# Performance work log

Measured on AMD Instinct MI355X. Metric: run time of the kernel, lower is better.

Reference implementation:

```python
import jax, jax.numpy as jnp
import numpy as np

N_NODES = 50000
N_EDGES = 800000
D_IN = 128
HIDDEN = 128
N_LAYERS = 3
N_CLASSES = 10
N_GRAPHS = 512
BN_EPS = 1e-5


def gcn_conv(x, edges, W, b):
    """PyG GCNConv: D^{-1/2}(A+I)D^{-1/2} X W + b (self-loops added)."""
    N = x.shape[0]
    src, dst = edges[0], edges[1]
    # degrees with self-loops
    deg = jax.ops.segment_sum(jnp.ones(src.shape[0], x.dtype), dst, num_segments=N) + 1.0
    dinv = jax.lax.rsqrt(deg)
    h = x @ W                                   # [N, out]
    norm = dinv[src] * dinv[dst]                # [E]
    out = jax.ops.segment_sum(h[src] * norm[:, None], dst, num_segments=N)
    out = out + h * (dinv * dinv)[:, None]      # self-loop messages
    return out + b


def batch_norm(x, gamma, beta):
    # BatchNorm1d in training mode: batch stats over node axis, biased var
    mu = x.mean(axis=0)
    var = x.var(axis=0)
    return gamma * (x - mu) * jax.lax.rsqrt(var + BN_EPS) + beta


def setup_inputs() -> dict:
    key = jax.random.key(0)
    ks = jax.random.split(key, 12)
    x = jax.random.normal(ks[0], (N_NODES, D_IN), dtype=jnp.float32)
    edges = jax.random.randint(ks[1], (2, N_EDGES), 0, N_NODES, dtype=jnp.int64)
    batch = jnp.sort(jax.random.randint(ks[2], (N_NODES,), 0, N_GRAPHS, dtype=jnp.int64))
    s_in = 1.0 / np.sqrt(D_IN)
    s_h = 1.0 / np.sqrt(HIDDEN)
    return {
        "x": x,
        "edges": edges,
        "batch": batch,
        "W1": jax.random.normal(ks[3], (D_IN, HIDDEN), dtype=jnp.float32) * s_in,
        "b1": jnp.zeros((HIDDEN,), jnp.float32),
        "g1": jnp.ones((HIDDEN,), jnp.float32),
        "be1": jnp.zeros((HIDDEN,), jnp.float32),
        "Wc": jax.random.normal(ks[4], (N_LAYERS, HIDDEN, HIDDEN), dtype=jnp.float32) * s_h,
        "bc": jnp.zeros((N_LAYERS, HIDDEN), jnp.float32),
        "gc": jnp.ones((N_LAYERS, HIDDEN), jnp.float32),
        "bec": jnp.zeros((N_LAYERS, HIDDEN), jnp.float32),
        "Wl": jax.random.normal(ks[5], (HIDDEN, N_CLASSES), dtype=jnp.float32) * s_h,
        "bl": jnp.zeros((N_CLASSES,), jnp.float32),
    }


def reference(x, edges, batch, W1, b1, g1, be1, Wc, bc, gc, bec, Wl, bl):
    h = jax.nn.relu(batch_norm(gcn_conv(x, edges, W1, b1), g1, be1))
    for i in range(N_LAYERS):  # fixed small layer loop
        h = jax.nn.relu(batch_norm(gcn_conv(h, edges, Wc[i], bc[i]), gc[i], bec[i]))
    # global_mean_pool over per-node graph ids
    sums = jax.ops.segment_sum(h, batch, num_segments=N_GRAPHS)
    counts = jax.ops.segment_sum(jnp.ones(h.shape[0], h.dtype), batch, num_segments=N_GRAPHS)
    pooled = sums / jnp.maximum(counts, 1.0)[:, None]
    return pooled @ Wl + bl
```

## Files before the change

kernel.cpp:

```cpp
#include <hip/hip_runtime.h>
#include <hip/hip_bf16.h>

#define NN 50000
#define NE 800000
#define DH 128
#define NGRAPH 512
#define NCLS 10
#define BN_EPS 1e-5f
#define SCAN_NB ((NN + 255) / 256)
#define GEMM_NB ((NN + 63) / 64)
#define BN1_NB 1024
#define BN2_NB 32
#define FILL_SEG 392
#define FILL_NB (FILL_SEG * 8)
#define STRIPE ((NN + 7) / 8)

typedef unsigned int uint;
typedef unsigned short ushort;
typedef __attribute__((ext_vector_type(8))) short short8;
typedef __attribute__((ext_vector_type(4))) float f32x4;

__device__ __forceinline__ ushort f2bf(float x) {
    __hip_bfloat16 h = __float2bfloat16(x);
    return *(ushort*)&h;
}
__device__ __forceinline__ float bf_lo(uint v) { return __uint_as_float(v << 16); }
__device__ __forceinline__ float bf_hi(uint v) { return __uint_as_float(v & 0xffff0000u); }


__launch_bounds__(256)
__global__ void hist_kernel(const int* __restrict__ dst, int* __restrict__ counts, int E) {
    int stripe = blockIdx.x & 7;
    int seg = blockIdx.x >> 3;
    int lo = stripe * STRIPE;
    int hi = lo + STRIPE;
    for (int e = seg * 256 + threadIdx.x; e < E; e += FILL_SEG * 256) {
        int d = dst[e];
        if (d >= lo && d < hi) atomicAdd(&counts[d], 1);
    }
}

__launch_bounds__(256)
__global__ void scan1_kernel(const int* __restrict__ counts, int* __restrict__ bsum, int N) {
    __shared__ int ls[256];
    int i = blockIdx.x * 256 + threadIdx.x;
    ls[threadIdx.x] = (i < N) ? counts[i] : 0;
    __syncthreads();
    for (int off = 128; off > 0; off >>= 1) {
        if (threadIdx.x < off) ls[threadIdx.x] += ls[threadIdx.x + off];
        __syncthreads();
    }
    if (threadIdx.x == 0) bsum[blockIdx.x] = ls[0];
}

__launch_bounds__(256)
__global__ void scan2_kernel(int* __restrict__ bsum, int NB) {
    __shared__ int ls[256];
    int tid = threadIdx.x;
    int v = (tid < NB) ? bsum[tid] : 0;
    ls[tid] = v;
    __syncthreads();
    for (int off = 1; off < 256; off <<= 1) {
        int t = (tid >= off) ? ls[tid - off] : 0;
        __syncthreads();
        ls[tid] += t;
        __syncthreads();
    }
    if (tid < NB) bsum[tid] = ls[tid] - v;
}

__launch_bounds__(256)
__global__ void scan3_kernel(const int* __restrict__ counts, const int* __restrict__ boff,
                             int* __restrict__ offsets, int* __restrict__ cursor,
                             float* __restrict__ dinv, int N) {
    __shared__ int ls[256];
    int tid = threadIdx.x;
    int i = blockIdx.x * 256 + tid;
    int v = (i < N) ? counts[i] : 0;
    ls[tid] = v;
    __syncthreads();
    for (int off = 1; off < 256; off <<= 1) {
        int t = (tid >= off) ? ls[tid - off] : 0;
        __syncthreads();
        ls[tid] += t;
        __syncthreads();
    }
    int base = boff[blockIdx.x];
    if (i < N) {
        int ex = base + ls[tid] - v;
        offsets[i] = ex;
        cursor[i] = ex;
        dinv[i] = rsqrtf((float)(v + 1));
        if (i == N - 1) offsets[N] = base + ls[tid];
    }
}

__launch_bounds__(256)
__global__ void fill_kernel(const int* __restrict__ src, const int* __restrict__ dst,
                            int* __restrict__ cursor, int* __restrict__ csr_src, int E) {
    int stripe = blockIdx.x & 7;
    int seg = blockIdx.x >> 3;
    int lo = stripe * STRIPE;
    int hi = lo + STRIPE;
    for (int e = seg * 256 + threadIdx.x; e < E; e += FILL_SEG * 256) {
        int d = dst[e];
        if (d >= lo && d < hi) {
            int pos = atomicAdd(&cursor[d], 1);
            csr_src[pos] = src[e];
        }
    }
}


__launch_bounds__(256)
__global__ void wtrans_kernel(const float* __restrict__ W1, const float* __restrict__ Wc,
                              ushort* __restrict__ WT) {
    int layer = blockIdx.x >> 4;
    int kt = (blockIdx.x >> 2) & 3, nt = blockIdx.x & 3;
    const float* W = (layer == 0) ? W1 : Wc + (size_t)(layer - 1) * DH * DH;
    __shared__ float tile[32][33];
    int t = threadIdx.x;
    int r = t >> 3;
    int c4 = (t & 7) * 4;
    float4 v = *(const float4*)&W[(size_t)(kt * 32 + r) * DH + nt * 32 + c4];
    tile[r][c4 + 0] = v.x; tile[r][c4 + 1] = v.y;
    tile[r][c4 + 2] = v.z; tile[r][c4 + 3] = v.w;
    __syncthreads();
    int n = t >> 3, k4 = (t & 7) * 4;
    ushort4 o;
    o.x = f2bf(tile[k4 + 0][n]);
    o.y = f2bf(tile[k4 + 1][n]);
    o.z = f2bf(tile[k4 + 2][n]);
    o.w = f2bf(tile[k4 + 3][n]);
    *(ushort4*)&WT[(size_t)layer * DH * DH + (size_t)(nt * 32 + n) * DH + kt * 32 + k4] = o;
}


template<int MODE>
__launch_bounds__(256)
__global__ void gemm_kernel(const float* __restrict__ Xf, const uint* __restrict__ Xb,
                            const ushort* __restrict__ WTl,
                            const float* __restrict__ bnacc, const float* __restrict__ gamma,
                            const float* __restrict__ beta, const float* __restrict__ dinv,
                            ushort* __restrict__ H, int N) {
    __shared__ uint4 xs4[64 * 16];
    __shared__ uint4 wt4[128 * 16];
    int t = threadIdx.x;
    int kc = t & 15;
    int row0 = blockIdx.x * 64;

    float sc[8], sh[8];
    if (MODE) {
        const float invN = 1.0f / (float)NN;
        #pragma unroll
        for (int j = 0; j < 8; j++) {
            int f = kc * 8 + j;
            float mean = bnacc[f] * invN;
            float var = bnacc[128 + f] * invN - mean * mean;
            float s = gamma[f] * rsqrtf(var + BN_EPS);
            sc[j] = s;
            sh[j] = beta[f] - mean * s;
        }
    }

    #pragma unroll
    for (int i = 0; i < 4; i++) {
        int row = (t >> 4) + i * 16;
        int r = row0 + row;
        float v[8];
        if (r < N) {
            if (MODE) {
                uint4 raw = ((const uint4*)Xb)[(size_t)r * 16 + kc];
                v[0] = bf_lo(raw.x); v[1] = bf_hi(raw.x);
                v[2] = bf_lo(raw.y); v[3] = bf_hi(raw.y);
                v[4] = bf_lo(raw.z); v[5] = bf_hi(raw.z);
                v[6] = bf_lo(raw.w); v[7] = bf_hi(raw.w);
                #pragma unroll
                for (int j = 0; j < 8; j++) v[j] = fmaxf(v[j] * sc[j] + sh[j], 0.f);
            } else {
                float4 a = ((const float4*)Xf)[(size_t)r * 32 + kc * 2];
                float4 b = ((const float4*)Xf)[(size_t)r * 32 + kc * 2 + 1];
                v[0] = a.x; v[1] = a.y; v[2] = a.z; v[3] = a.w;
                v[4] = b.x; v[5] = b.y; v[6] = b.z; v[7] = b.w;
            }
        } else {
            #pragma unroll
            for (int j = 0; j < 8; j++) v[j] = 0.f;
        }
        uint4 p;
        p.x = (uint)f2bf(v[0]) | ((uint)f2bf(v[1]) << 16);
        p.y = (uint)f2bf(v[2]) | ((uint)f2bf(v[3]) << 16);
        p.z = (uint)f2bf(v[4]) | ((uint)f2bf(v[5]) << 16);
        p.w = (uint)f2bf(v[6]) | ((uint)f2bf(v[7]) << 16);
        xs4[row * 16 + (kc ^ (row & 7))] = p;
    }
    const uint4* WT4 = (const uint4*)WTl;
    #pragma unroll
    for (int i = 0; i < 8; i++) {
        int n = (t >> 4) + i * 16;
        wt4[n * 16 + (kc ^ (n & 7))] = WT4[n * 16 + kc];
    }
    __syncthreads();

    int w = t >> 6, l = t & 63;
    int l16 = l >> 4;
    int lrow = w * 16 + (l & 15);
    f32x4 acc[8];
    #pragma unroll
    for (int c = 0; c < 8; c++) acc[c] = (f32x4){0.f, 0.f, 0.f, 0.f};

    #pragma unroll
    for (int ks = 0; ks < 4; ks++) {
        int kk = ks * 4 + l16;
        uint4 av = xs4[lrow * 16 + (kk ^ (lrow & 7))];
        short8 a = *(short8*)&av;
        #pragma unroll
        for (int c = 0; c < 8; c++) {
            int n = c * 16 + (l & 15);
            uint4 bv = wt4[n * 16 + (kk ^ (n & 7))];
            short8 b = *(short8*)&bv;
            acc[c] = __builtin_amdgcn_mfma_f32_16x16x32_bf16(a, b, acc[c], 0, 0, 0);
        }
    }

    #pragma unroll
    for (int j = 0; j < 4; j++) {
        int grow = row0 + w * 16 + l16 * 4 + j;
        if (grow < N) {
            float dv = dinv[grow];
            #pragma unroll
            for (int c = 0; c < 8; c++) {
                H[(size_t)grow * DH + c * 16 + (l & 15)] = f2bf(acc[c][j] * dv);
            }
        }
    }
}


__launch_bounds__(256)
__global__ void agg_kernel(const uint* __restrict__ H, const int* __restrict__ offsets,
                           const int* __restrict__ csr_src, const float* __restrict__ dinv,
                           const float* __restrict__ bias, uint* __restrict__ out, int N) {
    int n = blockIdx.x * 4 + (threadIdx.x >> 6);
    int lane = threadIdx.x & 63;
    if (n >= N) return;
    int beg = offsets[n], end = offsets[n + 1];
    float ax = 0.f, ay = 0.f;
    for (int e = beg; e < end; e += 8) {
        uint v[8];
        #pragma unroll
        for (int i = 0; i < 8; i++) {
            int ee = e + i;
            int sraw = csr_src[ee];
            int s = (ee < end) ? sraw : n;
            v[i] = H[(size_t)s * 64 + lane];
        }
        #pragma unroll
        for (int i = 0; i < 8; i++) {
            uint vv = (e + i < end) ? v[i] : 0u;
            ax += bf_lo(vv);
            ay += bf_hi(vv);
        }
    }
    uint vn = H[(size_t)n * 64 + lane];
    ax += bf_lo(vn);
    ay += bf_hi(vn);
    float dv = dinv[n];
    float2 b = ((const float2*)bias)[lane];
    float ox = ax * dv + b.x;
    float oy = ay * dv + b.y;
    out[(size_t)n * 64 + lane] = (uint)f2bf(ox) | ((uint)f2bf(oy) << 16);
}


__launch_bounds__(256)
__global__ void bnstats1_kernel(const uint* __restrict__ A, float* __restrict__ part, int N) {
    int u = threadIdx.x & 63;
    int rh = threadIdx.x >> 6;
    float slo = 0.f, shi = 0.f, qlo = 0.f, qhi = 0.f;
    for (int r = blockIdx.x * 4 + rh; r < N; r += BN1_NB * 4) {
        uint v = A[(size_t)r * 64 + u];
        float lo = bf_lo(v), hi = bf_hi(v);
        slo += lo; shi += hi;
        qlo += lo * lo; qhi += hi * hi;
    }
    __shared__ float4 red[4][64];
    red[rh][u] = make_float4(slo, shi, qlo, qhi);
    __syncthreads();
    if (threadIdx.x < 64) {
        float4 a = red[0][u], b = red[1][u], c = red[2][u], d = red[3][u];
        float* p = part + (size_t)blockIdx.x * 256;
        p[2 * u]           = a.x + b.x + c.x + d.x;
        p[2 * u + 1]       = a.y + b.y + c.y + d.y;
        p[128 + 2 * u]     = a.z + b.z + c.z + d.z;
        p[128 + 2 * u + 1] = a.w + b.w + c.w + d.w;
    }
}

__launch_bounds__(256)
__global__ void bnstats2_kernel(const float* __restrict__ part, float* __restrict__ acc) {
    int rows = BN1_NB / BN2_NB;
    float s = 0.f;
    int r0 = blockIdx.x * rows;
    for (int r = r0; r < r0 + rows; r++) s += part[(size_t)r * 256 + threadIdx.x];
    atomicAdd(&acc[threadIdx.x], s);
}


__device__ __forceinline__ int lower_bound_dev(const int* __restrict__ a, int n, int key) {
    int lo = 0, hi = n;
    while (lo < hi) {
        int m = (lo + hi) >> 1;
        if (a[m] < key) lo = m + 1; else hi = m;
    }
    return lo;
}

__launch_bounds__(256)
__global__ void pool_kernel(const uint* __restrict__ AGG, const int* __restrict__ batch,
                            const float* __restrict__ bnacc, const float* __restrict__ gamma,
                            const float* __restrict__ beta, float* __restrict__ pooled, int N) {
    int g = blockIdx.x;
    __shared__ int sbeg, send;
    if (threadIdx.x == 0) {
        sbeg = lower_bound_dev(batch, N, g);
        send = lower_bound_dev(batch, N, g + 1);
    }
    __syncthreads();
    int beg = sbeg, end = send;
    int u = threadIdx.x & 63;
    int rh = threadIdx.x >> 6;
    const float invN = 1.0f / (float)NN;
    float m0 = bnacc[2 * u] * invN,     m1 = bnacc[2 * u + 1] * invN;
    float v0 = bnacc[128 + 2 * u] * invN - m0 * m0;
    float v1 = bnacc[128 + 2 * u + 1] * invN - m1 * m1;
    float sc0 = gamma[2 * u] * rsqrtf(v0 + BN_EPS);
    float sc1 = gamma[2 * u + 1] * rsqrtf(v1 + BN_EPS);
    float sh0 = beta[2 * u] - m0 * sc0;
    float sh1 = beta[2 * u + 1] - m1 * sc1;
    float s0 = 0.f, s1 = 0.f;
    for (int r = beg + rh; r < end; r += 4) {
        uint v = AGG[(size_t)r * 64 + u];
        s0 += fmaxf(bf_lo(v) * sc0 + sh0, 0.f);
        s1 += fmaxf(bf_hi(v) * sc1 + sh1, 0.f);
    }
    __shared__ float2 ls[4][64];
    ls[rh][u] = make_float2(s0, s1);
    __syncthreads();
    if (threadIdx.x < 64) {
        float2 a = ls[0][u], b = ls[1][u], c = ls[2][u], d = ls[3][u];
        float cnt = fmaxf((float)(end - beg), 1.f);
        pooled[g * DH + 2 * u]     = (a.x + b.x + c.x + d.x) / cnt;
        pooled[g * DH + 2 * u + 1] = (a.y + b.y + c.y + d.y) / cnt;
    }
}


__launch_bounds__(256)
__global__ void final_kernel(const float* __restrict__ pooled, const float* __restrict__ Wl,
                             const float* __restrict__ bl, float* __restrict__ out) {
    int gid = blockIdx.x * blockDim.x + threadIdx.x;
    if (gid >= NGRAPH * NCLS) return;
    int g = gid / NCLS, c = gid % NCLS;
    float s = bl[c];
    #pragma unroll 8
    for (int k = 0; k < DH; k++) s += pooled[g * DH + k] * Wl[k * NCLS + c];
    out[gid] = s;
}


extern "C" void kernel_launch(void* const* d_in, const int* in_sizes, int n_in,
                              void* d_out, int out_size, void* d_ws, size_t ws_size,
                              hipStream_t stream) {
    const float* x     = (const float*)d_in[0];
    const int*   edges = (const int*)d_in[1];
    const int*   batch = (const int*)d_in[2];
    const float* W1    = (const float*)d_in[3];
    const float* b1    = (const float*)d_in[4];
    const float* g1    = (const float*)d_in[5];
    const float* be1   = (const float*)d_in[6];
    const float* Wc    = (const float*)d_in[7];
    const float* bc    = (const float*)d_in[8];
    const float* gc    = (const float*)d_in[9];
    const float* bec   = (const float*)d_in[10];
    const float* Wl    = (const float*)d_in[11];
    const float* bl    = (const float*)d_in[12];
    float* out = (float*)d_out;

    const int* esrc = edges;
    const int* edst = edges + NE;

    char* w = (char*)d_ws;
    auto alloc = [&](size_t bytes) -> void* {
        void* p = (void*)w;
        w += (bytes + 255) & ~(size_t)255;
        return p;
    };
    int*    counts  = (int*)alloc(NN * 4);
    int*    offsets = (int*)alloc((NN + 1) * 4);
    int*    cursor  = (int*)alloc(NN * 4);
    float*  dinv    = (float*)alloc(NN * 4);
    int*    csr_src = (int*)alloc(NE * 4 + 64);
    int*    bsum    = (int*)alloc(256 * 4);
    float*  bn_acc  = (float*)alloc(4 * 256 * 4);
    float*  bn_part = (float*)alloc((size_t)BN1_NB * 256 * 4);
    float*  pooled  = (float*)alloc(NGRAPH * DH * 4);
    ushort* WT      = (ushort*)alloc(4 * DH * DH * 2);
    uint*   H       = (uint*)alloc((size_t)NN * 64 * 4);
    uint*   AGG     = (uint*)alloc((size_t)NN * 64 * 4);

    hipMemsetAsync(counts, 0, NN * 4, stream);
    hipMemsetAsync(bn_acc, 0, 4 * 256 * 4, stream);
    hist_kernel<<<FILL_NB, 256, 0, stream>>>(edst, counts, NE);
    scan1_kernel<<<SCAN_NB, 256, 0, stream>>>(counts, bsum, NN);
    scan2_kernel<<<1, 256, 0, stream>>>(bsum, SCAN_NB);
    scan3_kernel<<<SCAN_NB, 256, 0, stream>>>(counts, bsum, offsets, cursor, dinv, NN);
    fill_kernel<<<FILL_NB, 256, 0, stream>>>(esrc, edst, cursor, csr_src, NE);
    wtrans_kernel<<<64, 256, 0, stream>>>(W1, Wc, WT);

    for (int l = 0; l < 4; l++) {
        const float* bm  = (l == 0) ? b1 : bc + (size_t)(l - 1) * DH;
        const float* gp  = (l == 1) ? g1 : gc + (size_t)(l - 2) * DH;
        const float* bep = (l == 1) ? be1 : bec + (size_t)(l - 2) * DH;
        const ushort* WTl = WT + (size_t)l * DH * DH;

        if (l == 0) {
            gemm_kernel<0><<<GEMM_NB, 256, 0, stream>>>(
                x, nullptr, WTl, nullptr, nullptr, nullptr, dinv, (ushort*)H, NN);
        } else {
            gemm_kernel<1><<<GEMM_NB, 256, 0, stream>>>(
                nullptr, AGG, WTl, bn_acc + (size_t)(l - 1) * 256, gp, bep, dinv,
                (ushort*)H, NN);
        }
        agg_kernel<<<(NN + 3) / 4, 256, 0, stream>>>(H, offsets, csr_src, dinv, bm, AGG, NN);
        bnstats1_kernel<<<BN1_NB, 256, 0, stream>>>(AGG, bn_part, NN);
        bnstats2_kernel<<<BN2_NB, 256, 0, stream>>>(bn_part, bn_acc + (size_t)l * 256);
    }

    pool_kernel<<<NGRAPH, 256, 0, stream>>>(AGG, batch, bn_acc + 3 * 256,
                                            gc + 2 * DH, bec + 2 * DH, pooled, NN);
    final_kernel<<<(NGRAPH * NCLS + 255) / 256, 256, 0, stream>>>(pooled, Wl, bl, out);
}
```

Before: 324.6 us.

## Fuse BatchNorm statistics into aggregation kernel via slotted atomics

Computes per-feature sum and sum-of-squares directly in the aggregation kernel from the values it just produced. Each block reduces its four rows in shared memory and atomically adds into one of 64 partial slots. A single-block reduce kernel then sums the slots and zeroes them for the next layer. This removes a full re-read of the aggregated activation array and one kernel launch per layer, at the cost of float atomic contention and a bounds check that now relies on NN being divisible by 4.

```diff
diff --git a/kernel.cpp b/kernel.cpp
--- a/kernel.cpp
+++ b/kernel.cpp
@@ -9,11 +9,10 @@
 #define BN_EPS 1e-5f
 #define SCAN_NB ((NN + 255) / 256)
 #define GEMM_NB ((NN + 63) / 64)
-#define BN1_NB 1024
-#define BN2_NB 32
 #define FILL_SEG 392
 #define FILL_NB (FILL_SEG * 8)
 #define STRIPE ((NN + 7) / 8)
+#define BN_SLOTS 64
 
 typedef unsigned int uint;
 typedef unsigned short ushort;
@@ -240,10 +239,11 @@
 __launch_bounds__(256)
 __global__ void agg_kernel(const uint* __restrict__ H, const int* __restrict__ offsets,
                            const int* __restrict__ csr_src, const float* __restrict__ dinv,
-                           const float* __restrict__ bias, uint* __restrict__ out, int N) {
-    int n = blockIdx.x * 4 + (threadIdx.x >> 6);
+                           const float* __restrict__ bias, uint* __restrict__ out,
+                           float* __restrict__ bn_part, int N) {
+    int wave = threadIdx.x >> 6;
     int lane = threadIdx.x & 63;
-    if (n >= N) return;
+    int n = blockIdx.x * 4 + wave;
     int beg = offsets[n], end = offsets[n + 1];
     float ax = 0.f, ay = 0.f;
     for (int e = beg; e < end; e += 8) {
@@ -270,40 +270,29 @@
     float ox = ax * dv + b.x;
     float oy = ay * dv + b.y;
     out[(size_t)n * 64 + lane] = (uint)f2bf(ox) | ((uint)f2bf(oy) << 16);
-}
-
-
-__launch_bounds__(256)
-__global__ void bnstats1_kernel(const uint* __restrict__ A, float* __restrict__ part, int N) {
-    int u = threadIdx.x & 63;
-    int rh = threadIdx.x >> 6;
-    float slo = 0.f, shi = 0.f, qlo = 0.f, qhi = 0.f;
-    for (int r = blockIdx.x * 4 + rh; r < N; r += BN1_NB * 4) {
-        uint v = A[(size_t)r * 64 + u];
-        float lo = bf_lo(v), hi = bf_hi(v);
-        slo += lo; shi += hi;
-        qlo += lo * lo; qhi += hi * hi;
-    }
+
     __shared__ float4 red[4][64];
-    red[rh][u] = make_float4(slo, shi, qlo, qhi);
+    red[wave][lane] = make_float4(ox, oy, ox * ox, oy * oy);
     __syncthreads();
     if (threadIdx.x < 64) {
-        float4 a = red[0][u], b = red[1][u], c = red[2][u], d = red[3][u];
-        float* p = part + (size_t)blockIdx.x * 256;
-        p[2 * u]           = a.x + b.x + c.x + d.x;
-        p[2 * u + 1]       = a.y + b.y + c.y + d.y;
-        p[128 + 2 * u]     = a.z + b.z + c.z + d.z;
-        p[128 + 2 * u + 1] = a.w + b.w + c.w + d.w;
-    }
-}
-
-__launch_bounds__(256)
-__global__ void bnstats2_kernel(const float* __restrict__ part, float* __restrict__ acc) {
-    int rows = BN1_NB / BN2_NB;
+        float4 a = red[0][lane], b1 = red[1][lane], c = red[2][lane], d = red[3][lane];
+        float* p = bn_part + (size_t)(blockIdx.x & (BN_SLOTS - 1)) * 256;
+        atomicAdd(&p[2 * lane],           a.x + b1.x + c.x + d.x);
+        atomicAdd(&p[2 * lane + 1],       a.y + b1.y + c.y + d.y);
+        atomicAdd(&p[128 + 2 * lane],     a.z + b1.z + c.z + d.z);
+        atomicAdd(&p[128 + 2 * lane + 1], a.w + b1.w + c.w + d.w);
+    }
+}
+
+__launch_bounds__(256)
+__global__ void bnreduce_kernel(float* __restrict__ part, float* __restrict__ acc) {
+    int t = threadIdx.x;
     float s = 0.f;
-    int r0 = blockIdx.x * rows;
-    for (int r = r0; r < r0 + rows; r++) s += part[(size_t)r * 256 + threadIdx.x];
-    atomicAdd(&acc[threadIdx.x], s);
+    #pragma unroll 8
+    for (int r = 0; r < BN_SLOTS; r++) s += part[(size_t)r * 256 + t];
+    acc[t] = s;
+    #pragma unroll 8
+    for (int r = 0; r < BN_SLOTS; r++) part[(size_t)r * 256 + t] = 0.f;
 }
 
 
@@ -403,14 +392,14 @@
     int*    csr_src = (int*)alloc(NE * 4 + 64);
     int*    bsum    = (int*)alloc(256 * 4);
     float*  bn_acc  = (float*)alloc(4 * 256 * 4);
-    float*  bn_part = (float*)alloc((size_t)BN1_NB * 256 * 4);
+    float*  bn_part = (float*)alloc((size_t)BN_SLOTS * 256 * 4);
     float*  pooled  = (float*)alloc(NGRAPH * DH * 4);
     ushort* WT      = (ushort*)alloc(4 * DH * DH * 2);
     uint*   H       = (uint*)alloc((size_t)NN * 64 * 4);
     uint*   AGG     = (uint*)alloc((size_t)NN * 64 * 4);
 
     hipMemsetAsync(counts, 0, NN * 4, stream);
-    hipMemsetAsync(bn_acc, 0, 4 * 256 * 4, stream);
+    hipMemsetAsync(bn_part, 0, (size_t)BN_SLOTS * 256 * 4, stream);
     hist_kernel<<<FILL_NB, 256, 0, stream>>>(edst, counts, NE);
     scan1_kernel<<<SCAN_NB, 256, 0, stream>>>(counts, bsum, NN);
     scan2_kernel<<<1, 256, 0, stream>>>(bsum, SCAN_NB);
@@ -432,9 +421,9 @@
                 nullptr, AGG, WTl, bn_acc + (size_t)(l - 1) * 256, gp, bep, dinv,
                 (ushort*)H, NN);
         }
-        agg_kernel<<<(NN + 3) / 4, 256, 0, stream>>>(H, offsets, csr_src, dinv, bm, AGG, NN);
-        bnstats1_kernel<<<BN1_NB, 256, 0, stream>>>(AGG, bn_part, NN);
-        bnstats2_kernel<<<BN2_NB, 256, 0, stream>>>(bn_part, bn_acc + (size_t)l * 256);
+        agg_kernel<<<NN / 4, 256, 0, stream>>>(H, offsets, csr_src, dinv, bm, AGG,
+                                               bn_part, NN);
+        bnreduce_kernel<<<1, 256, 0, stream>>>(bn_part, bn_acc + (size_t)l * 256);
     }
 
     pool_kernel<<<NGRAPH, 256, 0, stream>>>(AGG, batch, bn_acc + 3 * 256,
```

Measured after the change: 358.9 us. 10.6% more time.
